# Performance work log

Measured on AMD Instinct MI355X. Metric: run time of the kernel, lower is better.

The kernel has to match this reference:

```python
import jax, jax.numpy as jnp
import numpy as np

H, W, A, C = 200, 704, 2, 256   # BEV grid, anchors, feature channels
NC, K = 4, 20000                # peer CAVs, selected anchors per CAV
REG = 7 * A                     # reg head channels


def setup_inputs() -> dict:
    key = jax.random.key(0)
    ks = jax.random.split(key, 8)
    feat = jax.random.normal(ks[0], (1, C, H, W), jnp.float32)
    cls_w = jax.random.normal(ks[1], (A, C), jnp.float32) * 0.02
    cls_b = jnp.zeros((A,), jnp.float32)
    reg_w = jax.random.normal(ks[2], (REG, C), jnp.float32) * 0.02
    reg_b = jnp.zeros((REG,), jnp.float32)
    psm_v2x = jax.random.normal(ks[3], (NC, K), jnp.float32)
    rm_v2x = jax.random.normal(ks[4], (NC, 7 * K), jnp.float32)
    scores_v2x = jax.random.uniform(ks[5], (NC, K), jnp.float32, 0.3, 1.0)
    flat = A * H * W
    idx = []
    for i in range(NC):  # unique sorted flat indices per CAV (masked_select semantics)
        perm = jax.random.permutation(jax.random.fold_in(ks[6], i), flat)[:K]
        idx.append(jnp.sort(perm))
    mask_idx = jnp.stack(idx).astype(jnp.int32)
    # mask_reg = mask.repeat(1,7,1,1): indices tile with offsets r*A*H*W
    offs = (jnp.arange(7) * flat).astype(jnp.int32)
    mask_reg_idx = (mask_idx[:, None, :] + offs[None, :, None]).reshape(NC, 7 * K)
    return {
        'spatial_features_2d': feat, 'cls_w': cls_w, 'cls_b': cls_b,
        'reg_w': reg_w, 'reg_b': reg_b, 'psm_v2x': psm_v2x, 'rm_v2x': rm_v2x,
        'scores_v2x': scores_v2x, 'mask_idx': mask_idx, 'mask_reg_idx': mask_reg_idx,
    }


def _restore(vals, idx, shape):
    # restore_tensor: scatter compacted values into zeros at flat indices, per CAV
    n = vals.shape[0]
    flat = int(np.prod(shape))
    out = jnp.zeros((n, flat), vals.dtype)
    out = out.at[jnp.arange(n)[:, None], idx].set(vals)
    return out.reshape((n,) + shape)


def reference(spatial_features_2d, cls_w, cls_b, reg_w, reg_b,
              psm_v2x, rm_v2x, scores_v2x, mask_idx, mask_reg_idx):
    # 1x1 conv heads
    psm_single = jnp.einsum('bchw,ac->bahw', spatial_features_2d, cls_w) + cls_b[None, :, None, None]
    rm_single = jnp.einsum('bchw,rc->brhw', spatial_features_2d, reg_w) + reg_b[None, :, None, None]
    prob = jax.nn.sigmoid(psm_single)
    # scatter-restore peer CAV results onto the BEV grid
    r_psm = _restore(psm_v2x, mask_idx, (A, H, W))        # [NC,A,H,W]
    r_scores = _restore(scores_v2x, mask_idx, (A, H, W))
    r_rm = _restore(rm_v2x, mask_reg_idx, (REG, H, W))    # [NC,14,H,W]
    psm_all = jnp.concatenate([psm_single, r_psm], axis=0)      # [1+NC,A,H,W]
    prob_all = jnp.concatenate([prob, r_scores], axis=0)
    rm_all = jnp.concatenate([rm_single, r_rm], axis=0)         # [1+NC,14,H,W]
    # per-cell winning CAV by score, then gather psm/rm from the winner
    cav = jnp.argmax(prob_all, axis=0)                    # [A,H,W]
    psm = jnp.take_along_axis(psm_all, cav[None], axis=0) # [1,A,H,W]
    cav_reg = jnp.tile(cav, (7, 1, 1))                    # [14,H,W]
    rm = jnp.take_along_axis(rm_all, cav_reg[None], axis=0)  # [1,14,H,W]
    return psm, rm
```

## Files before the change

kernel.cpp:

```cpp
#include <hip/hip_runtime.h>

#define HH 200
#define WW 704
#define HW (HH * WW)
#define HW2 (HW / 2)
#define AHW (2 * HW)
#define CC 256
#define NCAV 4
#define KK 20000
#define NJ 16
#define UPIPE 8
#define CPW 64

typedef unsigned int u32;

__global__ void scatter_best(const int* __restrict__ mask_idx,
                             const float* __restrict__ scores,
                             u32* __restrict__ winmap) {
    int t = blockIdx.x * blockDim.x + threadIdx.x;
    if (t >= NCAV * KK) return;
    int x = mask_idx[t];
    int n = t / KK;
    union { float f; u32 u; } s;
    s.f = scores[t];
    u32 pack = ((s.u - 0x3E800000u) << 7) | (u32)(3 - n);
    atomicMax(winmap + x, pack);
}

__device__ __forceinline__ int bsearch_row(const int* __restrict__ row, int x) {
    int lo = 0, hi = KK;
    while (lo < hi) {
        int mid = (lo + hi) >> 1;
        if (row[mid] < x) lo = mid + 1; else hi = mid;
    }
    return lo;
}

__global__ __launch_bounds__(256, 4) void head_select(
    const float2* __restrict__ feat2,
    const float* __restrict__ cls_w,
    const float* __restrict__ reg_w,
    const float* __restrict__ cls_b,
    const float* __restrict__ reg_b,
    const float* __restrict__ psm_v2x,
    const float* __restrict__ rm_v2x,
    const int* __restrict__ mask_idx,
    const u32* __restrict__ winmap,
    float* __restrict__ out) {
    __shared__ float smem[8192];

    int tid = threadIdx.x;
    int w = tid >> 6, lane = tid & 63;

    for (int i = tid; i < CC * NJ; i += 256) {
        int j = i >> 8, c = i & 255;
        smem[c * NJ + j] = (j < 2) ? cls_w[j * CC + c] : reg_w[(j - 2) * CC + c];
    }
    __syncthreads();

    int q = blockIdx.x * 64 + lane;
    const float2* fp = feat2 + q + (size_t)(w * CPW) * HW2;

    float acc[2][NJ];
#pragma unroll
    for (int j = 0; j < NJ; ++j) { acc[0][j] = 0.0f; acc[1][j] = 0.0f; }

    float2 A[UPIPE], B[UPIPE];
#pragma unroll
    for (int u = 0; u < UPIPE; ++u) A[u] = fp[u * HW2];

    for (int cb = 0; cb < CPW; cb += 2 * UPIPE) {
#pragma unroll
        for (int u = 0; u < UPIPE; ++u) B[u] = fp[(cb + UPIPE + u) * HW2];
#pragma unroll
        for (int u = 0; u < UPIPE; ++u) {
            const float4* wv = (const float4*)&smem[(w * CPW + cb + u) * NJ];
            float wt[NJ];
            *(float4*)&wt[0]  = wv[0];
            *(float4*)&wt[4]  = wv[1];
            *(float4*)&wt[8]  = wv[2];
            *(float4*)&wt[12] = wv[3];
#pragma unroll
            for (int j = 0; j < NJ; ++j) {
                acc[0][j] += A[u].x * wt[j];
                acc[1][j] += A[u].y * wt[j];
            }
        }
#pragma unroll
        for (int u = 0; u < UPIPE; ++u) {
            int cn = cb + 2 * UPIPE + u;
            A[u] = fp[(cn < CPW ? cn : 0) * HW2];
        }
#pragma unroll
        for (int u = 0; u < UPIPE; ++u) {
            const float4* wv = (const float4*)&smem[(w * CPW + cb + UPIPE + u) * NJ];
            float wt[NJ];
            *(float4*)&wt[0]  = wv[0];
            *(float4*)&wt[4]  = wv[1];
            *(float4*)&wt[8]  = wv[2];
            *(float4*)&wt[12] = wv[3];
#pragma unroll
            for (int j = 0; j < NJ; ++j) {
                acc[0][j] += B[u].x * wt[j];
                acc[1][j] += B[u].y * wt[j];
            }
        }
    }
    __syncthreads();

#pragma unroll
    for (int e = 0; e < 2; ++e)
#pragma unroll
        for (int j = 0; j < NJ; ++j)
            smem[(e * NJ + j) * 256 + tid] = acc[e][j];
    __syncthreads();

    if (tid < 128) {
        int g = tid >> 1, e = tid & 1;
        int p = blockIdx.x * 128 + tid;
        float val[NJ];
#pragma unroll
        for (int j = 0; j < NJ; ++j) {
            float b = (j < 2) ? cls_b[j] : reg_b[j - 2];
            float s = b;
#pragma unroll
            for (int wv = 0; wv < 4; ++wv)
                s += smem[(e * NJ + j) * 256 + wv * 64 + g];
            val[j] = s;
        }
#pragma unroll
        for (int a = 0; a < 2; ++a) {
            float pv = val[a];
            float prob = 1.0f / (1.0f + expf(-pv));
            int x = a * HW + p;
            u32 win = winmap[x];
            float sc = 0.0f;
            if (win != 0u) {
                union { u32 u; float f; } v;
                v.u = (win >> 7) + 0x3E800000u;
                sc = v.f;
            }
            if (sc > prob) {
                int n = 3 - (int)(win & 3u);
                int k = bsearch_row(mask_idx + n * KK, x);
                out[x] = psm_v2x[n * KK + k];
#pragma unroll
                for (int r = 0; r < 7; ++r)
                    out[AHW + (2 * r + a) * HW + p] =
                        rm_v2x[n * (7 * KK) + r * KK + k];
            } else {
                out[x] = pv;
#pragma unroll
                for (int r = 0; r < 7; ++r)
                    out[AHW + (2 * r + a) * HW + p] = val[2 + 2 * r + a];
            }
        }
    }
}

extern "C" void kernel_launch(void* const* d_in, const int* in_sizes, int n_in,
                              void* d_out, int out_size, void* d_ws, size_t ws_size,
                              hipStream_t stream) {
    const float* feat    = (const float*)d_in[0];
    const float* cls_w   = (const float*)d_in[1];
    const float* cls_b   = (const float*)d_in[2];
    const float* reg_w   = (const float*)d_in[3];
    const float* reg_b   = (const float*)d_in[4];
    const float* psm_v2x = (const float*)d_in[5];
    const float* rm_v2x  = (const float*)d_in[6];
    const float* scores  = (const float*)d_in[7];
    const int* mask_idx  = (const int*)d_in[8];

    const size_t win_bytes = (size_t)AHW * sizeof(u32);
    u32* winmap = (ws_size >= win_bytes) ? (u32*)d_ws : (u32*)d_in[9];

    hipMemsetAsync(winmap, 0, win_bytes, stream);

    scatter_best<<<(NCAV * KK + 255) / 256, 256, 0, stream>>>(mask_idx, scores, winmap);
    head_select<<<HW2 / 64, 256, 0, stream>>>(
        (const float2*)feat, cls_w, reg_w, cls_b, reg_b,
        psm_v2x, rm_v2x, mask_idx, winmap, (float*)d_out);
}
```

Before: 250.2 us.

## Stage feature loads through LDS with direct global-to-LDS copies

Replaces the register double-buffered float2 feature loads with __builtin_amdgcn_global_load_lds, which copies 16-byte chunks per lane straight into a per-wave shared-memory staging area in batches of 16 channels, then reads float2 values from LDS for the FMA loop. The aim is wider, more efficient global loads and fewer VGPRs spent on in-flight prefetch registers. In exchange, shared memory grows to 48KB, launch bounds drop to 3 blocks per CU, and each batch waits on a full vmcnt drain with no overlap between loading and computing. Adds the risk that the raw waitcnt encoding is wrong.

```diff
diff --git a/kernel.cpp b/kernel.cpp
--- a/kernel.cpp
+++ b/kernel.cpp
@@ -3,14 +3,13 @@
 #define HH 200
 #define WW 704
 #define HW (HH * WW)
-#define HW2 (HW / 2)
 #define AHW (2 * HW)
 #define CC 256
 #define NCAV 4
 #define KK 20000
 #define NJ 16
-#define UPIPE 8
 #define CPW 64
+#define BCH 16
 
 typedef unsigned int u32;
 
@@ -36,8 +35,8 @@
     return lo;
 }
 
-__global__ __launch_bounds__(256, 4) void head_select(
-    const float2* __restrict__ feat2,
+__global__ __launch_bounds__(256, 3) void head_select(
+    const float* __restrict__ feat,
     const float* __restrict__ cls_w,
     const float* __restrict__ reg_w,
     const float* __restrict__ cls_b,
@@ -47,7 +46,7 @@
     const int* __restrict__ mask_idx,
     const u32* __restrict__ winmap,
     float* __restrict__ out) {
-    __shared__ float smem[8192];
+    __shared__ float smem[12288];
 
     int tid = threadIdx.x;
     int w = tid >> 6, lane = tid & 63;
@@ -58,51 +57,39 @@
     }
     __syncthreads();
 
-    int q = blockIdx.x * 64 + lane;
-    const float2* fp = feat2 + q + (size_t)(w * CPW) * HW2;
-
     float acc[2][NJ];
 #pragma unroll
     for (int j = 0; j < NJ; ++j) { acc[0][j] = 0.0f; acc[1][j] = 0.0f; }
 
-    float2 A[UPIPE], B[UPIPE];
+    int half = lane >> 5, sub = lane & 31;
+    const float* gbase = feat + (size_t)blockIdx.x * 128 + sub * 4;
+    float* stage = &smem[4096 + w * 2048];
+
+    for (int b = 0; b < CPW / BCH; ++b) {
+        int cb = w * CPW + b * BCH;
 #pragma unroll
-    for (int u = 0; u < UPIPE; ++u) A[u] = fp[u * HW2];
-
-    for (int cb = 0; cb < CPW; cb += 2 * UPIPE) {
+        for (int i = 0; i < BCH / 2; ++i) {
+            const float* gp = gbase + (size_t)(cb + 2 * i + half) * HW;
+            __builtin_amdgcn_global_load_lds(
+                (const __attribute__((address_space(1))) void*)gp,
+                (__attribute__((address_space(3))) void*)(stage + i * 256),
+                16, 0, 0);
+        }
+        __builtin_amdgcn_s_waitcnt(0x0F70);
+        __builtin_amdgcn_wave_barrier();
 #pragma unroll
-        for (int u = 0; u < UPIPE; ++u) B[u] = fp[(cb + UPIPE + u) * HW2];
-#pragma unroll
-        for (int u = 0; u < UPIPE; ++u) {
-            const float4* wv = (const float4*)&smem[(w * CPW + cb + u) * NJ];
+        for (int cl = 0; cl < BCH; ++cl) {
+            const float4* wv = (const float4*)&smem[(cb + cl) * NJ];
             float wt[NJ];
             *(float4*)&wt[0]  = wv[0];
             *(float4*)&wt[4]  = wv[1];
             *(float4*)&wt[8]  = wv[2];
             *(float4*)&wt[12] = wv[3];
+            float2 f = *(const float2*)&stage[cl * 128 + lane * 2];
 #pragma unroll
             for (int j = 0; j < NJ; ++j) {
-                acc[0][j] += A[u].x * wt[j];
-                acc[1][j] += A[u].y * wt[j];
-            }
-        }
-#pragma unroll
-        for (int u = 0; u < UPIPE; ++u) {
-            int cn = cb + 2 * UPIPE + u;
-            A[u] = fp[(cn < CPW ? cn : 0) * HW2];
-        }
-#pragma unroll
-        for (int u = 0; u < UPIPE; ++u) {
-            const float4* wv = (const float4*)&smem[(w * CPW + cb + UPIPE + u) * NJ];
-            float wt[NJ];
-            *(float4*)&wt[0]  = wv[0];
-            *(float4*)&wt[4]  = wv[1];
-            *(float4*)&wt[8]  = wv[2];
-            *(float4*)&wt[12] = wv[3];
-#pragma unroll
-            for (int j = 0; j < NJ; ++j) {
-                acc[0][j] += B[u].x * wt[j];
-                acc[1][j] += B[u].y * wt[j];
+                acc[0][j] += f.x * wt[j];
+                acc[1][j] += f.y * wt[j];
             }
         }
     }
@@ -121,8 +108,7 @@
         float val[NJ];
 #pragma unroll
         for (int j = 0; j < NJ; ++j) {
-            float b = (j < 2) ? cls_b[j] : reg_b[j - 2];
-            float s = b;
+            float s = (j < 2) ? cls_b[j] : reg_b[j - 2];
 #pragma unroll
             for (int wv = 0; wv < 4; ++wv)
                 s += smem[(e * NJ + j) * 256 + wv * 64 + g];
@@ -177,7 +163,7 @@
     hipMemsetAsync(winmap, 0, win_bytes, stream);
 
     scatter_best<<<(NCAV * KK + 255) / 256, 256, 0, stream>>>(mask_idx, scores, winmap);
-    head_select<<<HW2 / 64, 256, 0, stream>>>(
-        (const float2*)feat, cls_w, reg_w, cls_b, reg_b,
+    head_select<<<HW / 128, 256, 0, stream>>>(
+        feat, cls_w, reg_w, cls_b, reg_b,
         psm_v2x, rm_v2x, mask_idx, winmap, (float*)d_out);
 }
```

Measured after the change: 253.3 us. No clear change (+1.2%).
